# Kernel optimization log

Hardware: AMD Instinct MI355X
Metric: run time of the kernel (lower is better)

## Reference

```python
import jax, jax.numpy as jnp
import numpy as np

NUM_EXPERTS = 64
TOP_K = 8
NORM_TOPK_PROB = True


def setup_inputs() -> dict:
    key = jax.random.key(0)
    k1, k2 = jax.random.split(key)
    hidden_states = jax.random.normal(k1, (8192, 4096), dtype=jnp.float32)
    gate_w = jax.random.normal(k2, (NUM_EXPERTS, 4096), dtype=jnp.float32) * (1.0 / np.sqrt(4096))
    return {"hidden_states": hidden_states, "gate_w": gate_w}


def reference(hidden_states, gate_w):
    # router_logits: (T, E) = hidden @ gate_w.T
    router_logits = jnp.einsum('th,eh->te', hidden_states, gate_w)
    # softmax in float32 (matches F.softmax(..., dtype=torch.float32))
    router_probs = jax.nn.softmax(router_logits.astype(jnp.float32), axis=-1)
    # top-k selection (descending, like torch.topk)
    expert_weights, expert_indices = jax.lax.top_k(router_probs, TOP_K)
    if NORM_TOPK_PROB:
        expert_weights = expert_weights / jnp.sum(expert_weights, axis=-1, keepdims=True)
    expert_weights = expert_weights.astype(hidden_states.dtype)
    # load-balancing loss: N_e * sum_i f_i * p_i
    num_tokens = router_probs.shape[0]
    one_hot = jax.nn.one_hot(expert_indices, NUM_EXPERTS, dtype=jnp.float32)  # (T, K, E)
    tokens_per_expert = one_hot.sum(axis=(0, 1))                              # (E,)
    f = tokens_per_expert / (num_tokens * TOP_K)
    p = router_probs.mean(axis=0)
    aux_loss = NUM_EXPERTS * jnp.sum(f * p)
    return (expert_weights, expert_indices, aux_loss)
```

## Files before the change

kernel.cpp:

```cpp
#include <hip/hip_runtime.h>
#include <math.h>

#define HDIM 4096
#define NEXP 64
#define NTOK 8192
#define KSPLIT 8
#define KSLICE (HDIM / KSPLIT)
#define BM 128
#define CHUNK 32
#define NCHUNK (KSLICE / CHUNK)
#define ASTRIDE 40
#define SLICEOFF 1024
#define TPW 2

typedef short short8 __attribute__((ext_vector_type(8)));
typedef float f32x4 __attribute__((ext_vector_type(4)));

__device__ __forceinline__ void split2x3(float x0, float x1, int& h, int& md, int& lo) {
  unsigned u0 = __float_as_uint(x0), u1 = __float_as_uint(x1);
  unsigned h0 = u0 & 0xFFFF0000u, h1 = u1 & 0xFFFF0000u;
  float r0 = x0 - __uint_as_float(h0);
  float r1 = x1 - __uint_as_float(h1);
  unsigned m0 = __float_as_uint(r0) & 0xFFFF0000u;
  unsigned m1 = __float_as_uint(r1) & 0xFFFF0000u;
  float s0 = r0 - __uint_as_float(m0);
  float s1 = r1 - __uint_as_float(m1);
  h  = (int)((h0 >> 16) | h1);
  md = (int)((m0 >> 16) | m1);
  lo = (int)((__float_as_uint(s0) >> 16) | (__float_as_uint(s1) & 0xFFFF0000u));
}

__global__ __launch_bounds__(256, 3) void gemm_k(const float* __restrict__ A,
                                                 const float* __restrict__ W,
                                                 float* __restrict__ Lp,
                                                 int atomic_mode) {
  __shared__ __align__(16) short Ah[BM * ASTRIDE], Amid[BM * ASTRIDE], Alo[BM * ASTRIDE];
  __shared__ __align__(16) short Bh[NEXP * ASTRIDE], Bmid[NEXP * ASTRIDE], Blo[NEXP * ASTRIDE];
  const int tid = threadIdx.x;
  const int m_base = blockIdx.x * BM;
  const int k_base = blockIdx.y * KSLICE;
  float* Lout = Lp + (atomic_mode ? (size_t)0 : (size_t)blockIdx.y * NTOK * NEXP);

  const int srow = tid >> 2;
  const int skg = tid & 3;
  const float* gA0 = A + (size_t)(m_base + srow) * HDIM + k_base + skg * 8;
  const float* gA1 = gA0 + (size_t)64 * HDIM;
  const float* gB = W + (size_t)srow * HDIM + k_base + skg * 8;

  const int lane = tid & 63;
  const int wave = tid >> 6;
  const int l15 = lane & 15;
  const int quad = lane >> 4;
  const int wm = wave * 32;

  f32x4 acc[2][4];
#pragma unroll
  for (int mt = 0; mt < 2; ++mt)
#pragma unroll
    for (int nt = 0; nt < 4; ++nt) acc[mt][nt] = (f32x4){0.f, 0.f, 0.f, 0.f};

  float4 pa0[2], pa1[2], pb[2];
  auto gload = [&](int i) {
    const float* p = gA0 + i * CHUNK;
    pa0[0] = *(const float4*)(p);
    pa0[1] = *(const float4*)(p + 4);
    p = gA1 + i * CHUNK;
    pa1[0] = *(const float4*)(p);
    pa1[1] = *(const float4*)(p + 4);
    p = gB + i * CHUNK;
    pb[0] = *(const float4*)(p);
    pb[1] = *(const float4*)(p + 4);
  };
  auto convert_store = [&]() {
    const float fa0[8] = {pa0[0].x, pa0[0].y, pa0[0].z, pa0[0].w,
                          pa0[1].x, pa0[1].y, pa0[1].z, pa0[1].w};
    const float fa1[8] = {pa1[0].x, pa1[0].y, pa1[0].z, pa1[0].w,
                          pa1[1].x, pa1[1].y, pa1[1].z, pa1[1].w};
    const float fb[8] = {pb[0].x, pb[0].y, pb[0].z, pb[0].w,
                         pb[1].x, pb[1].y, pb[1].z, pb[1].w};
    int h[4], md[4], lo[4];
    int off = srow * ASTRIDE + skg * 8;
#pragma unroll
    for (int j = 0; j < 4; ++j) split2x3(fa0[2 * j], fa0[2 * j + 1], h[j], md[j], lo[j]);
    *(int4*)&Ah[off] = make_int4(h[0], h[1], h[2], h[3]);
    *(int4*)&Amid[off] = make_int4(md[0], md[1], md[2], md[3]);
    *(int4*)&Alo[off] = make_int4(lo[0], lo[1], lo[2], lo[3]);
#pragma unroll
    for (int j = 0; j < 4; ++j) split2x3(fa1[2 * j], fa1[2 * j + 1], h[j], md[j], lo[j]);
    int off1 = (srow + 64) * ASTRIDE + skg * 8;
    *(int4*)&Ah[off1] = make_int4(h[0], h[1], h[2], h[3]);
    *(int4*)&Amid[off1] = make_int4(md[0], md[1], md[2], md[3]);
    *(int4*)&Alo[off1] = make_int4(lo[0], lo[1], lo[2], lo[3]);
#pragma unroll
    for (int j = 0; j < 4; ++j) split2x3(fb[2 * j], fb[2 * j + 1], h[j], md[j], lo[j]);
    *(int4*)&Bh[off] = make_int4(h[0], h[1], h[2], h[3]);
    *(int4*)&Bmid[off] = make_int4(md[0], md[1], md[2], md[3]);
    *(int4*)&Blo[off] = make_int4(lo[0], lo[1], lo[2], lo[3]);
  };

  gload(0);
  convert_store();
  __syncthreads();

  for (int i = 0; i < NCHUNK; ++i) {
    if (i + 1 < NCHUNK) gload(i + 1);
    short8 fa[2][3];
#pragma unroll
    for (int mt = 0; mt < 2; ++mt) {
      const int r = (wm + mt * 16 + l15) * ASTRIDE + quad * 8;
      fa[mt][0] = *(const short8*)&Ah[r];
      fa[mt][1] = *(const short8*)&Amid[r];
      fa[mt][2] = *(const short8*)&Alo[r];
    }
#pragma unroll
    for (int nt = 0; nt < 4; ++nt) {
      const int r = (nt * 16 + l15) * ASTRIDE + quad * 8;
      const short8 bh = *(const short8*)&Bh[r];
      const short8 bm = *(const short8*)&Bmid[r];
      const short8 bl = *(const short8*)&Blo[r];
#pragma unroll
      for (int mt = 0; mt < 2; ++mt) {
        f32x4 c = acc[mt][nt];
        c = __builtin_amdgcn_mfma_f32_16x16x32_bf16(fa[mt][0], bh, c, 0, 0, 0);
        c = __builtin_amdgcn_mfma_f32_16x16x32_bf16(fa[mt][0], bm, c, 0, 0, 0);
        c = __builtin_amdgcn_mfma_f32_16x16x32_bf16(fa[mt][1], bh, c, 0, 0, 0);
        c = __builtin_amdgcn_mfma_f32_16x16x32_bf16(fa[mt][0], bl, c, 0, 0, 0);
        c = __builtin_amdgcn_mfma_f32_16x16x32_bf16(fa[mt][2], bh, c, 0, 0, 0);
        c = __builtin_amdgcn_mfma_f32_16x16x32_bf16(fa[mt][1], bm, c, 0, 0, 0);
        acc[mt][nt] = c;
      }
    }
    __syncthreads();
    if (i + 1 < NCHUNK) convert_store();
    __syncthreads();
  }

#pragma unroll
  for (int mt = 0; mt < 2; ++mt)
#pragma unroll
    for (int nt = 0; nt < 4; ++nt)
#pragma unroll
      for (int r = 0; r < 4; ++r) {
        const int m = m_base + wm + mt * 16 + quad * 4 + r;
        const int n = nt * 16 + l15;
        if (atomic_mode) atomicAdd(&Lout[(size_t)m * NEXP + n], acc[mt][nt][r]);
        else Lout[(size_t)m * NEXP + n] = acc[mt][nt][r];
      }
}

__global__ __launch_bounds__(256) void topk_k(const float* __restrict__ Lp, int nsl,
                                              float* __restrict__ out,
                                              float* __restrict__ auxbuf) {
  __shared__ float sl[4][64];
  __shared__ float s_aux[128];
  const int tid = threadIdx.x;
  const int wave = tid >> 6, lane = tid & 63;
  if (tid < 128) s_aux[tid] = 0.f;
  __syncthreads();

  for (int it = 0; it < TPW; ++it) {
    const int t = (blockIdx.x * 4 + wave) * TPW + it;
    float x = 0.f;
    for (int s = 0; s < nsl; ++s)
      x += Lp[(size_t)s * (NTOK * NEXP) + (size_t)t * NEXP + lane];
    sl[wave][lane] = x;

    float mx = x;
#pragma unroll
    for (int off = 32; off >= 1; off >>= 1)
      mx = fmaxf(mx, __shfl_xor(mx, off, 64));
    const float e = __expf(x - mx);
    float ssum = e;
#pragma unroll
    for (int off = 32; off >= 1; off >>= 1) ssum += __shfl_xor(ssum, off, 64);
    const float prob = e / ssum;

    __syncthreads();

    int cnt = 0;
#pragma unroll
    for (int c = 0; c < 4; ++c) {
      const float4 v0 = *(const float4*)&sl[wave][c * 16 + 0];
      const float4 v1 = *(const float4*)&sl[wave][c * 16 + 4];
      const float4 v2 = *(const float4*)&sl[wave][c * 16 + 8];
      const float4 v3 = *(const float4*)&sl[wave][c * 16 + 12];
      const float xv[16] = {v0.x, v0.y, v0.z, v0.w, v1.x, v1.y, v1.z, v1.w,
                            v2.x, v2.y, v2.z, v2.w, v3.x, v3.y, v3.z, v3.w};
#pragma unroll
      for (int j = 0; j < 16; ++j) {
        const int jj = c * 16 + j;
        cnt += (xv[j] > x) || (xv[j] == x && jj < lane);
      }
    }

    float tp = (cnt < 8) ? prob : 0.f;
    float tsum = tp;
#pragma unroll
    for (int off = 32; off >= 1; off >>= 1) tsum += __shfl_xor(tsum, off, 64);

    const int dst = cnt << 2;
    const float pv = __uint_as_float(
        (unsigned)__builtin_amdgcn_ds_permute(dst, (int)__float_as_uint(prob)));
    const int pi = __builtin_amdgcn_ds_permute(dst, lane);
    if (lane < 8) {
      out[(size_t)t * 8 + lane] = pv / tsum;
      out[(size_t)NTOK * 8 + (size_t)t * 8 + lane] = (float)pi;
    }
    atomicAdd(&s_aux[lane], prob);
    if (cnt < 8) atomicAdd(&s_aux[64 + lane], 1.f);
  }
  __syncthreads();
  if (tid < 128) atomicAdd(&auxbuf[(blockIdx.x & 7) * 128 + tid], s_aux[tid]);
}

__global__ void aux_k(const float* __restrict__ auxbuf, float* __restrict__ out) {
  const int e = threadIdx.x;
  float p = 0.f, f = 0.f;
#pragma unroll
  for (int c = 0; c < 8; ++c) {
    p += auxbuf[c * 128 + e];
    f += auxbuf[c * 128 + 64 + e];
  }
  p *= (1.f / (float)NTOK);
  f *= (1.f / ((float)NTOK * 8.f));
  float v = f * p;
#pragma unroll
  for (int off = 32; off >= 1; off >>= 1) v += __shfl_xor(v, off, 64);
  if (e == 0) out[2 * NTOK * 8] = 64.f * v;
}

extern "C" void kernel_launch(void* const* d_in, const int* in_sizes, int n_in,
                              void* d_out, int out_size, void* d_ws, size_t ws_size,
                              hipStream_t stream) {
  const float* hidden = (const float*)d_in[0];
  const float* gate = (const float*)d_in[1];
  float* out = (float*)d_out;
  float* ws = (float*)d_ws;
  float* auxbuf = ws;
  float* slices = ws + SLICEOFF;

  const size_t need = (size_t)SLICEOFF * 4 + (size_t)KSPLIT * NTOK * NEXP * 4;
  const int atomic_mode = (ws_size < need) ? 1 : 0;
  const int nsl = atomic_mode ? 1 : KSPLIT;

  if (atomic_mode)
    hipMemsetAsync(d_ws, 0, (size_t)SLICEOFF * 4 + (size_t)NTOK * NEXP * 4, stream);
  else
    hipMemsetAsync(d_ws, 0, (size_t)SLICEOFF * 4, stream);

  gemm_k<<<dim3(64, KSPLIT), 256, 0, stream>>>(hidden, gate, slices, atomic_mode);
  topk_k<<<NTOK / (4 * TPW), 256, 0, stream>>>(slices, nsl, out, auxbuf);
  aux_k<<<1, 64, 0, stream>>>(auxbuf, out);
}
```

Baseline: 216.3 us.

## Pre-split gate weights in a prep kernel and drop LDS staging in GEMM

Adds a prep kernel that splits the gate weights once into bf16 hi/mid/lo terms, stored in an MFMA-fragment-friendly layout in workspace. The same kernel also zeroes the aux buffer, which replaces one memset. The GEMM now loads A straight from global memory into registers in fragment order, splits it in registers, and reads B fragments from global/L2 without shared memory or barriers. This removes LDS traffic and __syncthreads, but A loads become less coalesced (32-byte segments per lane) and it adds one extra kernel launch.

```diff
diff --git a/kernel.cpp b/kernel.cpp
--- a/kernel.cpp
+++ b/kernel.cpp
@@ -6,15 +6,17 @@
 #define NTOK 8192
 #define KSPLIT 8
 #define KSLICE (HDIM / KSPLIT)
-#define BM 128
-#define CHUNK 32
-#define NCHUNK (KSLICE / CHUNK)
-#define ASTRIDE 40
-#define SLICEOFF 1024
+#define NCHUNK (KSLICE / 32)
+#define NKC (HDIM / 32)
+#define AUXF 1024
 #define TPW 2
+#define BT_TERM (NKC * 4 * 64 * 8)
+#define BT_KC (4 * 64 * 8)
 
 typedef short short8 __attribute__((ext_vector_type(8)));
 typedef float f32x4 __attribute__((ext_vector_type(4)));
+
+union i4s8 { int4 i; short8 s; };
 
 __device__ __forceinline__ void split2x3(float x0, float x1, int& h, int& md, int& lo) {
   unsigned u0 = __float_as_uint(x0), u1 = __float_as_uint(x1);
@@ -30,28 +32,52 @@
   lo = (int)((__float_as_uint(s0) >> 16) | (__float_as_uint(s1) & 0xFFFF0000u));
 }
 
-__global__ __launch_bounds__(256, 3) void gemm_k(const float* __restrict__ A,
-                                                 const float* __restrict__ W,
-                                                 float* __restrict__ Lp,
-                                                 int atomic_mode) {
-  __shared__ __align__(16) short Ah[BM * ASTRIDE], Amid[BM * ASTRIDE], Alo[BM * ASTRIDE];
-  __shared__ __align__(16) short Bh[NEXP * ASTRIDE], Bmid[NEXP * ASTRIDE], Blo[NEXP * ASTRIDE];
+__device__ __forceinline__ void split8(const float4& p0, const float4& p1,
+                                       short8& h8, short8& m8, short8& l8) {
+  i4s8 h, m, l;
+  split2x3(p0.x, p0.y, h.i.x, m.i.x, l.i.x);
+  split2x3(p0.z, p0.w, h.i.y, m.i.y, l.i.y);
+  split2x3(p1.x, p1.y, h.i.z, m.i.z, l.i.z);
+  split2x3(p1.z, p1.w, h.i.w, m.i.w, l.i.w);
+  h8 = h.s; m8 = m.s; l8 = l.s;
+}
+
+__global__ __launch_bounds__(256) void prep_k(const float* __restrict__ W,
+                                              short* __restrict__ Bs,
+                                              float* __restrict__ auxbuf) {
+  if (blockIdx.x == 128) {
+#pragma unroll
+    for (int j = 0; j < 4; ++j) auxbuf[j * 256 + threadIdx.x] = 0.f;
+    return;
+  }
+  const int g = blockIdx.x * 256 + threadIdx.x;
+  const int n = g >> 9;
+  const int k8 = g & 511;
+  const float4 p0 = *(const float4*)&W[(size_t)n * HDIM + k8 * 8];
+  const float4 p1 = *(const float4*)&W[(size_t)n * HDIM + k8 * 8 + 4];
+  short8 h8, m8, l8;
+  split8(p0, p1, h8, m8, l8);
+  const int kc = k8 >> 2, quad = k8 & 3;
+  const size_t o = (((size_t)kc * 4 + quad) * 64 + n) * 8;
+  *(short8*)&Bs[o] = h8;
+  *(short8*)&Bs[o + BT_TERM] = m8;
+  *(short8*)&Bs[o + 2 * BT_TERM] = l8;
+}
+
+__global__ __launch_bounds__(256) void gemm_k(const float* __restrict__ A,
+                                              const short* __restrict__ Bs,
+                                              float* __restrict__ Lp,
+                                              int atomic_mode) {
   const int tid = threadIdx.x;
-  const int m_base = blockIdx.x * BM;
-  const int k_base = blockIdx.y * KSLICE;
-  float* Lout = Lp + (atomic_mode ? (size_t)0 : (size_t)blockIdx.y * NTOK * NEXP);
-
-  const int srow = tid >> 2;
-  const int skg = tid & 3;
-  const float* gA0 = A + (size_t)(m_base + srow) * HDIM + k_base + skg * 8;
-  const float* gA1 = gA0 + (size_t)64 * HDIM;
-  const float* gB = W + (size_t)srow * HDIM + k_base + skg * 8;
-
-  const int lane = tid & 63;
-  const int wave = tid >> 6;
-  const int l15 = lane & 15;
-  const int quad = lane >> 4;
-  const int wm = wave * 32;
+  const int wave = tid >> 6, lane = tid & 63;
+  const int l15 = lane & 15, quad = lane >> 4;
+  const int m_base = blockIdx.x * 128 + wave * 32;
+  const int kb = blockIdx.y;
+  float* Lout = Lp + (atomic_mode ? (size_t)0 : (size_t)kb * NTOK * NEXP);
+
+  const float* a0 = A + (size_t)(m_base + l15) * HDIM + kb * KSLICE + quad * 8;
+  const float* a1 = a0 + (size_t)16 * HDIM;
+  const short* bbase = Bs + ((size_t)(kb * NCHUNK) * 4 + quad) * 512 + l15 * 8;
 
   f32x4 acc[2][4];
 #pragma unroll
@@ -59,65 +85,29 @@
 #pragma unroll
     for (int nt = 0; nt < 4; ++nt) acc[mt][nt] = (f32x4){0.f, 0.f, 0.f, 0.f};
 
-  float4 pa0[2], pa1[2], pb[2];
-  auto gload = [&](int i) {
-    const float* p = gA0 + i * CHUNK;
-    pa0[0] = *(const float4*)(p);
-    pa0[1] = *(const float4*)(p + 4);
-    p = gA1 + i * CHUNK;
-    pa1[0] = *(const float4*)(p);
-    pa1[1] = *(const float4*)(p + 4);
-    p = gB + i * CHUNK;
-    pb[0] = *(const float4*)(p);
-    pb[1] = *(const float4*)(p + 4);
+  float4 ra[2][2][2];
+  auto loadA = [&](int buf, int i) {
+    ra[buf][0][0] = *(const float4*)(a0 + i * 32);
+    ra[buf][0][1] = *(const float4*)(a0 + i * 32 + 4);
+    ra[buf][1][0] = *(const float4*)(a1 + i * 32);
+    ra[buf][1][1] = *(const float4*)(a1 + i * 32 + 4);
   };
-  auto convert_store = [&]() {
-    const float fa0[8] = {pa0[0].x, pa0[0].y, pa0[0].z, pa0[0].w,
-                          pa0[1].x, pa0[1].y, pa0[1].z, pa0[1].w};
-    const float fa1[8] = {pa1[0].x, pa1[0].y, pa1[0].z, pa1[0].w,
-                          pa1[1].x, pa1[1].y, pa1[1].z, pa1[1].w};
-    const float fb[8] = {pb[0].x, pb[0].y, pb[0].z, pb[0].w,
-                         pb[1].x, pb[1].y, pb[1].z, pb[1].w};
-    int h[4], md[4], lo[4];
-    int off = srow * ASTRIDE + skg * 8;
-#pragma unroll
-    for (int j = 0; j < 4; ++j) split2x3(fa0[2 * j], fa0[2 * j + 1], h[j], md[j], lo[j]);
-    *(int4*)&Ah[off] = make_int4(h[0], h[1], h[2], h[3]);
-    *(int4*)&Amid[off] = make_int4(md[0], md[1], md[2], md[3]);
-    *(int4*)&Alo[off] = make_int4(lo[0], lo[1], lo[2], lo[3]);
-#pragma unroll
-    for (int j = 0; j < 4; ++j) split2x3(fa1[2 * j], fa1[2 * j + 1], h[j], md[j], lo[j]);
-    int off1 = (srow + 64) * ASTRIDE + skg * 8;
-    *(int4*)&Ah[off1] = make_int4(h[0], h[1], h[2], h[3]);
-    *(int4*)&Amid[off1] = make_int4(md[0], md[1], md[2], md[3]);
-    *(int4*)&Alo[off1] = make_int4(lo[0], lo[1], lo[2], lo[3]);
-#pragma unroll
-    for (int j = 0; j < 4; ++j) split2x3(fb[2 * j], fb[2 * j + 1], h[j], md[j], lo[j]);
-    *(int4*)&Bh[off] = make_int4(h[0], h[1], h[2], h[3]);
-    *(int4*)&Bmid[off] = make_int4(md[0], md[1], md[2], md[3]);
-    *(int4*)&Blo[off] = make_int4(lo[0], lo[1], lo[2], lo[3]);
-  };
-
-  gload(0);
-  convert_store();
-  __syncthreads();
-
+  loadA(0, 0);
+
+#pragma unroll 2
   for (int i = 0; i < NCHUNK; ++i) {
-    if (i + 1 < NCHUNK) gload(i + 1);
+    const int cur = i & 1;
+    if (i + 1 < NCHUNK) loadA(cur ^ 1, i + 1);
     short8 fa[2][3];
 #pragma unroll
-    for (int mt = 0; mt < 2; ++mt) {
-      const int r = (wm + mt * 16 + l15) * ASTRIDE + quad * 8;
-      fa[mt][0] = *(const short8*)&Ah[r];
-      fa[mt][1] = *(const short8*)&Amid[r];
-      fa[mt][2] = *(const short8*)&Alo[r];
-    }
+    for (int mt = 0; mt < 2; ++mt)
+      split8(ra[cur][mt][0], ra[cur][mt][1], fa[mt][0], fa[mt][1], fa[mt][2]);
+    const short* bc = bbase + (size_t)i * BT_KC;
 #pragma unroll
     for (int nt = 0; nt < 4; ++nt) {
-      const int r = (nt * 16 + l15) * ASTRIDE + quad * 8;
-      const short8 bh = *(const short8*)&Bh[r];
-      const short8 bm = *(const short8*)&Bmid[r];
-      const short8 bl = *(const short8*)&Blo[r];
+      const short8 bh = *(const short8*)(bc + nt * 128);
+      const short8 bm = *(const short8*)(bc + nt * 128 + BT_TERM);
+      const short8 bl = *(const short8*)(bc + nt * 128 + 2 * BT_TERM);
 #pragma unroll
       for (int mt = 0; mt < 2; ++mt) {
         f32x4 c = acc[mt][nt];
@@ -130,9 +120,6 @@
         acc[mt][nt] = c;
       }
     }
-    __syncthreads();
-    if (i + 1 < NCHUNK) convert_store();
-    __syncthreads();
   }
 
 #pragma unroll
@@ -141,7 +128,7 @@
     for (int nt = 0; nt < 4; ++nt)
 #pragma unroll
       for (int r = 0; r < 4; ++r) {
-        const int m = m_base + wm + mt * 16 + quad * 4 + r;
+        const int m = m_base + mt * 16 + quad * 4 + r;
         const int n = nt * 16 + l15;
         if (atomic_mode) atomicAdd(&Lout[(size_t)m * NEXP + n], acc[mt][nt][r]);
         else Lout[(size_t)m * NEXP + n] = acc[mt][nt][r];
@@ -237,18 +224,19 @@
   float* out = (float*)d_out;
   float* ws = (float*)d_ws;
   float* auxbuf = ws;
-  float* slices = ws + SLICEOFF;
-
-  const size_t need = (size_t)SLICEOFF * 4 + (size_t)KSPLIT * NTOK * NEXP * 4;
-  const int atomic_mode = (ws_size < need) ? 1 : 0;
+
+  const size_t full_need =
+      (size_t)AUXF * 4 + (size_t)KSPLIT * NTOK * NEXP * 4 + (size_t)3 * BT_TERM * 2;
+  const int atomic_mode = (ws_size < full_need) ? 1 : 0;
   const int nsl = atomic_mode ? 1 : KSPLIT;
+  float* slices = ws + AUXF;
+  short* Bs = (short*)(ws + AUXF + (size_t)nsl * NTOK * NEXP);
 
   if (atomic_mode)
-    hipMemsetAsync(d_ws, 0, (size_t)SLICEOFF * 4 + (size_t)NTOK * NEXP * 4, stream);
-  else
-    hipMemsetAsync(d_ws, 0, (size_t)SLICEOFF * 4, stream);
-
-  gemm_k<<<dim3(64, KSPLIT), 256, 0, stream>>>(hidden, gate, slices, atomic_mode);
+    hipMemsetAsync(slices, 0, (size_t)NTOK * NEXP * 4, stream);
+
+  prep_k<<<129, 256, 0, stream>>>(gate, Bs, auxbuf);
+  gemm_k<<<dim3(64, KSPLIT), 256, 0, stream>>>(hidden, Bs, slices, atomic_mode);
   topk_k<<<NTOK / (4 * TPW), 256, 0, stream>>>(slices, nsl, out, auxbuf);
   aux_k<<<1, 64, 0, stream>>>(auxbuf, out);
 }
```

New measurement: 227.8 us. +5.3%, slower.
